# Kernel tuning notes

Measured on AMD Instinct MI355X. Metric: run time of the kernel, lower is better.

Reference implementation:

```python
import jax, jax.numpy as jnp
import numpy as np

N = 100000
NODE_DIM = 128
HIDDEN_DIM = 64
E = 625000


def setup_inputs() -> dict:
    key = jax.random.key(0)
    k_x, k_e, k_w1, k_b1, k_w2, k_b2 = jax.random.split(key, 6)
    x = jax.random.normal(k_x, (N, NODE_DIM), dtype=jnp.float32)
    edge_index = jax.random.randint(k_e, (2, E), 0, N, dtype=jnp.int64)
    # nn.Linear default init: U(-1/sqrt(fan_in), 1/sqrt(fan_in))
    lim1 = 1.0 / np.sqrt(2 * NODE_DIM)
    W1 = jax.random.uniform(k_w1, (2 * NODE_DIM, HIDDEN_DIM), minval=-lim1, maxval=lim1, dtype=jnp.float32)
    b1 = jax.random.uniform(k_b1, (HIDDEN_DIM,), minval=-lim1, maxval=lim1, dtype=jnp.float32)
    lim2 = 1.0 / np.sqrt(HIDDEN_DIM)
    W2 = jax.random.uniform(k_w2, (HIDDEN_DIM, 1), minval=-lim2, maxval=lim2, dtype=jnp.float32)
    b2 = jax.random.uniform(k_b2, (1,), minval=-lim2, maxval=lim2, dtype=jnp.float32)
    return {"x": x, "edge_index": edge_index, "W1": W1, "b1": b1, "W2": W2, "b2": b2}


def reference(x, edge_index, W1, b1, W2, b2):
    row, col = edge_index[0], edge_index[1]
    # (E, 2*node_dim) gathered edge features
    edge_attr = jnp.concatenate([x[row], x[col]], axis=-1)
    h = jax.nn.relu(edge_attr @ W1 + b1)           # (E, hidden)
    edge_mask = jax.nn.sigmoid(h @ W2 + b2)[:, 0]  # (E,)
    return edge_mask
```

## Files before the change

kernel.cpp:

```cpp
#include <hip/hip_runtime.h>
#include <hip/hip_bf16.h>

typedef unsigned short u16x8 __attribute__((ext_vector_type(8)));
typedef __bf16 bf16x8 __attribute__((ext_vector_type(8)));
typedef float f32x4 __attribute__((ext_vector_type(4)));

#define NODE_DIM 128
#define LPAD 136

__device__ __forceinline__ unsigned short f2bf(float f) {
  union { float f; unsigned int u; } v; v.f = f;
  unsigned int u = v.u;
  u += 0x7fffu + ((u >> 16) & 1u);
  return (unsigned short)(u >> 16);
}
__device__ __forceinline__ float bf2f(unsigned short s) {
  union { unsigned int u; float f; } v; v.u = ((unsigned int)s) << 16;
  return v.f;
}

__global__ void prep_wt(const float* __restrict__ W1, unsigned short* __restrict__ Wt) {
  for (int i = blockIdx.x * blockDim.x + threadIdx.x; i < 128 * 128;
       i += gridDim.x * blockDim.x) {
    int j = i >> 7, k = i & 127;
    float w = (j < 64) ? W1[k * 64 + j] : W1[(k + 128) * 64 + (j - 64)];
    Wt[i] = f2bf(w);
  }
}

__global__ __launch_bounds__(256) void gemm_pq(const float* __restrict__ x,
                                               const unsigned short* __restrict__ Wt,
                                               unsigned short* __restrict__ PQ,
                                               int n_nodes) {
  __shared__ unsigned short bs[128][LPAD];
  const int tid = threadIdx.x;

  for (int i = tid; i < 128 * 16; i += 256) {
    int j = i >> 4, c = i & 15;
    *(u16x8*)&bs[j][c * 8] = *(const u16x8*)&Wt[j * 128 + c * 8];
  }
  __syncthreads();

  const int wave = tid >> 6, lane = tid & 63;
  const int m = lane & 15, q = lane >> 4;

  #pragma unroll
  for (int step = 0; step < 2; ++step) {
    const int row0 = blockIdx.x * 128 + step * 64 + wave * 16;
    if (row0 < n_nodes) {
      const int arow = min(row0 + m, n_nodes - 1);
      const float* xr = x + (size_t)arow * NODE_DIM;

      float4 av[4][2];
      #pragma unroll
      for (int kk = 0; kk < 4; kk++) {
        av[kk][0] = *(const float4*)&xr[kk * 32 + q * 8];
        av[kk][1] = *(const float4*)&xr[kk * 32 + q * 8 + 4];
      }

      f32x4 acc[8];
      #pragma unroll
      for (int t = 0; t < 8; t++) acc[t] = f32x4{0.f, 0.f, 0.f, 0.f};

      #pragma unroll
      for (int kk = 0; kk < 4; kk++) {
        union { unsigned short s[8]; u16x8 v; } au;
        au.s[0] = f2bf(av[kk][0].x); au.s[1] = f2bf(av[kk][0].y);
        au.s[2] = f2bf(av[kk][0].z); au.s[3] = f2bf(av[kk][0].w);
        au.s[4] = f2bf(av[kk][1].x); au.s[5] = f2bf(av[kk][1].y);
        au.s[6] = f2bf(av[kk][1].z); au.s[7] = f2bf(av[kk][1].w);
        bf16x8 a = __builtin_bit_cast(bf16x8, au.v);
        #pragma unroll
        for (int t = 0; t < 8; t++) {
          bf16x8 b = __builtin_bit_cast(bf16x8,
              *(const u16x8*)&bs[t * 16 + m][kk * 32 + q * 8]);
          acc[t] = __builtin_amdgcn_mfma_f32_16x16x32_bf16(a, b, acc[t], 0, 0, 0);
        }
      }

      #pragma unroll
      for (int t = 0; t < 8; t++) {
        #pragma unroll
        for (int r = 0; r < 4; r++) {
          int gr = row0 + q * 4 + r;
          if (gr < n_nodes) PQ[(size_t)gr * 128 + t * 16 + m] = f2bf(acc[t][r]);
        }
      }
    }
  }
}

__global__ __launch_bounds__(256) void edge_mlp(const int* __restrict__ ei,
                                                const unsigned short* __restrict__ PQ,
                                                const float* __restrict__ b1,
                                                const float* __restrict__ W2,
                                                const float* __restrict__ b2,
                                                float* __restrict__ out, int E) {
  const int t = blockIdx.x * 256 + threadIdx.x;
  const int e = t >> 3, l = t & 7;
  if (e >= E) return;
  const int row = ei[e];
  const int col = ei[E + e];
  u16x8 pu = *(const u16x8*)&PQ[(size_t)row * 128 + l * 8];
  u16x8 qu = *(const u16x8*)&PQ[(size_t)col * 128 + 64 + l * 8];
  float partial = 0.f;
  #pragma unroll
  for (int i = 0; i < 8; i++) {
    float h = bf2f(pu[i]) + bf2f(qu[i]) + b1[l * 8 + i];
    h = fmaxf(h, 0.f);
    partial = fmaf(h, W2[l * 8 + i], partial);
  }
  partial += __shfl_xor(partial, 1);
  partial += __shfl_xor(partial, 2);
  partial += __shfl_xor(partial, 4);
  if (l == 0) out[e] = 1.f / (1.f + __expf(-(partial + b2[0])));
}

extern "C" void kernel_launch(void* const* d_in, const int* in_sizes, int n_in,
                              void* d_out, int out_size, void* d_ws, size_t ws_size,
                              hipStream_t stream) {
  const float* x  = (const float*)d_in[0];
  const int*   ei = (const int*)d_in[1];
  const float* W1 = (const float*)d_in[2];
  const float* b1 = (const float*)d_in[3];
  const float* W2 = (const float*)d_in[4];
  const float* b2 = (const float*)d_in[5];
  float* out = (float*)d_out;
  const int n_nodes = in_sizes[0] / NODE_DIM;
  const int E = in_sizes[1] / 2;

  unsigned short* Wt = (unsigned short*)d_ws;
  unsigned short* PQ = (unsigned short*)((char*)d_ws + 32768);

  prep_wt<<<16, 256, 0, stream>>>(W1, Wt);
  gemm_pq<<<(n_nodes + 127) / 128, 256, 0, stream>>>(x, Wt, PQ, n_nodes);
  const int egrid = (E * 8 + 255) / 256;
  edge_mlp<<<egrid, 256, 0, stream>>>(ei, PQ, b1, W2, b2, out, E);
}
```

Before: 129.0 us.

## Fuse weight prep, node GEMM and edge MLP into one cooperative kernel

Replaces the three separate launches with a single persistent cooperative kernel of 512 blocks. The phases are separated by grid-wide syncs, and the work uses grid-stride loops over node tiles and edges. This removes per-launch overhead and the idle gaps between kernels. In exchange it adds grid.sync costs and limits parallelism to a fixed resident grid, which may lower memory-level parallelism. The original three-kernel path stays as a fallback if the cooperative launch fails.

```diff
diff --git a/kernel.cpp b/kernel.cpp
--- a/kernel.cpp
+++ b/kernel.cpp
@@ -1,5 +1,8 @@
 #include <hip/hip_runtime.h>
 #include <hip/hip_bf16.h>
+#include <hip/hip_cooperative_groups.h>
+
+namespace cg = cooperative_groups;
 
 typedef unsigned short u16x8 __attribute__((ext_vector_type(8)));
 typedef __bf16 bf16x8 __attribute__((ext_vector_type(8)));
@@ -7,6 +10,7 @@
 
 #define NODE_DIM 128
 #define LPAD 136
+#define GRID_BLKS 512
 
 __device__ __forceinline__ unsigned short f2bf(float f) {
   union { float f; unsigned int u; } v; v.f = f;
@@ -17,6 +21,100 @@
 __device__ __forceinline__ float bf2f(unsigned short s) {
   union { unsigned int u; float f; } v; v.u = ((unsigned int)s) << 16;
   return v.f;
+}
+
+__global__ __launch_bounds__(256, 2) void fused(
+    const float* __restrict__ x, const int* __restrict__ ei,
+    const float* __restrict__ W1, const float* __restrict__ b1,
+    const float* __restrict__ W2, const float* __restrict__ b2,
+    float* __restrict__ out, unsigned short* __restrict__ Wt,
+    unsigned short* __restrict__ PQ, int n_nodes, int E) {
+  __shared__ unsigned short bs[128][LPAD];
+  const int tid = threadIdx.x;
+  const int nthreads = gridDim.x * 256;
+  cg::grid_group grid = cg::this_grid();
+
+  for (int i = blockIdx.x * 256 + tid; i < 128 * 128; i += nthreads) {
+    int j = i >> 7, k = i & 127;
+    float w = (j < 64) ? W1[k * 64 + j] : W1[(k + 128) * 64 + (j - 64)];
+    Wt[i] = f2bf(w);
+  }
+  __threadfence();
+  grid.sync();
+
+  for (int i = tid; i < 128 * 16; i += 256) {
+    int j = i >> 4, c = i & 15;
+    *(u16x8*)&bs[j][c * 8] = *(const u16x8*)&Wt[j * 128 + c * 8];
+  }
+  __syncthreads();
+
+  const int wave = tid >> 6, lane = tid & 63;
+  const int m = lane & 15, q = lane >> 4;
+  const int ntiles = (n_nodes + 63) / 64;
+
+  for (int tile = blockIdx.x; tile < ntiles; tile += gridDim.x) {
+    const int row0 = tile * 64 + wave * 16;
+    const int arow = min(row0 + m, n_nodes - 1);
+    const float* xr = x + (size_t)arow * NODE_DIM;
+
+    float4 av[4][2];
+    #pragma unroll
+    for (int kk = 0; kk < 4; kk++) {
+      av[kk][0] = *(const float4*)&xr[kk * 32 + q * 8];
+      av[kk][1] = *(const float4*)&xr[kk * 32 + q * 8 + 4];
+    }
+
+    f32x4 acc[8];
+    #pragma unroll
+    for (int t = 0; t < 8; t++) acc[t] = f32x4{0.f, 0.f, 0.f, 0.f};
+
+    #pragma unroll
+    for (int kk = 0; kk < 4; kk++) {
+      union { unsigned short s[8]; u16x8 v; } au;
+      au.s[0] = f2bf(av[kk][0].x); au.s[1] = f2bf(av[kk][0].y);
+      au.s[2] = f2bf(av[kk][0].z); au.s[3] = f2bf(av[kk][0].w);
+      au.s[4] = f2bf(av[kk][1].x); au.s[5] = f2bf(av[kk][1].y);
+      au.s[6] = f2bf(av[kk][1].z); au.s[7] = f2bf(av[kk][1].w);
+      bf16x8 a = __builtin_bit_cast(bf16x8, au.v);
+      #pragma unroll
+      for (int t = 0; t < 8; t++) {
+        bf16x8 b = __builtin_bit_cast(bf16x8,
+            *(const u16x8*)&bs[t * 16 + m][kk * 32 + q * 8]);
+        acc[t] = __builtin_amdgcn_mfma_f32_16x16x32_bf16(a, b, acc[t], 0, 0, 0);
+      }
+    }
+
+    #pragma unroll
+    for (int t = 0; t < 8; t++) {
+      #pragma unroll
+      for (int r = 0; r < 4; r++) {
+        int gr = row0 + q * 4 + r;
+        if (gr < n_nodes) PQ[(size_t)gr * 128 + t * 16 + m] = f2bf(acc[t][r]);
+      }
+    }
+  }
+  __threadfence();
+  grid.sync();
+
+  const int l = tid & 7;
+  for (int idx = blockIdx.x * 256 + tid; (idx >> 3) < E; idx += nthreads) {
+    const int e = idx >> 3;
+    const int row = ei[e];
+    const int col = ei[E + e];
+    u16x8 pu = *(const u16x8*)&PQ[(size_t)row * 128 + l * 8];
+    u16x8 qu = *(const u16x8*)&PQ[(size_t)col * 128 + 64 + l * 8];
+    float partial = 0.f;
+    #pragma unroll
+    for (int i = 0; i < 8; i++) {
+      float h = bf2f(pu[i]) + bf2f(qu[i]) + b1[l * 8 + i];
+      h = fmaxf(h, 0.f);
+      partial = fmaf(h, W2[l * 8 + i], partial);
+    }
+    partial += __shfl_xor(partial, 1);
+    partial += __shfl_xor(partial, 2);
+    partial += __shfl_xor(partial, 4);
+    if (l == 0) out[e] = 1.f / (1.f + __expf(-(partial + b2[0])));
+  }
 }
 
 __global__ void prep_wt(const float* __restrict__ W1, unsigned short* __restrict__ Wt) {
@@ -34,34 +132,28 @@
                                                int n_nodes) {
   __shared__ unsigned short bs[128][LPAD];
   const int tid = threadIdx.x;
-
   for (int i = tid; i < 128 * 16; i += 256) {
     int j = i >> 4, c = i & 15;
     *(u16x8*)&bs[j][c * 8] = *(const u16x8*)&Wt[j * 128 + c * 8];
   }
   __syncthreads();
-
   const int wave = tid >> 6, lane = tid & 63;
   const int m = lane & 15, q = lane >> 4;
-
   #pragma unroll
   for (int step = 0; step < 2; ++step) {
     const int row0 = blockIdx.x * 128 + step * 64 + wave * 16;
     if (row0 < n_nodes) {
       const int arow = min(row0 + m, n_nodes - 1);
       const float* xr = x + (size_t)arow * NODE_DIM;
-
       float4 av[4][2];
       #pragma unroll
       for (int kk = 0; kk < 4; kk++) {
         av[kk][0] = *(const float4*)&xr[kk * 32 + q * 8];
         av[kk][1] = *(const float4*)&xr[kk * 32 + q * 8 + 4];
       }
-
       f32x4 acc[8];
       #pragma unroll
       for (int t = 0; t < 8; t++) acc[t] = f32x4{0.f, 0.f, 0.f, 0.f};
-
       #pragma unroll
       for (int kk = 0; kk < 4; kk++) {
         union { unsigned short s[8]; u16x8 v; } au;
@@ -77,7 +169,6 @@
           acc[t] = __builtin_amdgcn_mfma_f32_16x16x32_bf16(a, b, acc[t], 0, 0, 0);
         }
       }
-
       #pragma unroll
       for (int t = 0; t < 8; t++) {
         #pragma unroll
@@ -126,14 +217,21 @@
   const float* W2 = (const float*)d_in[4];
   const float* b2 = (const float*)d_in[5];
   float* out = (float*)d_out;
-  const int n_nodes = in_sizes[0] / NODE_DIM;
-  const int E = in_sizes[1] / 2;
+  int n_nodes = in_sizes[0] / NODE_DIM;
+  int E = in_sizes[1] / 2;
 
   unsigned short* Wt = (unsigned short*)d_ws;
   unsigned short* PQ = (unsigned short*)((char*)d_ws + 32768);
 
-  prep_wt<<<16, 256, 0, stream>>>(W1, Wt);
-  gemm_pq<<<(n_nodes + 127) / 128, 256, 0, stream>>>(x, Wt, PQ, n_nodes);
-  const int egrid = (E * 8 + 255) / 256;
-  edge_mlp<<<egrid, 256, 0, stream>>>(ei, PQ, b1, W2, b2, out, E);
-}
+  void* args[] = {(void*)&x, (void*)&ei, (void*)&W1, (void*)&b1, (void*)&W2,
+                  (void*)&b2, (void*)&out, (void*)&Wt, (void*)&PQ,
+                  (void*)&n_nodes, (void*)&E};
+  hipError_t err = hipLaunchCooperativeKernel(
+      reinterpret_cast<void*>(fused), dim3(GRID_BLKS), dim3(256), args, 0, stream);
+  if (err != hipSuccess) {
+    prep_wt<<<16, 256, 0, stream>>>(W1, Wt);
+    gemm_pq<<<(n_nodes + 127) / 128, 256, 0, stream>>>(x, Wt, PQ, n_nodes);
+    const int egrid = (E * 8 + 255) / 256;
+    edge_mlp<<<egrid, 256, 0, stream>>>(ei, PQ, b1, W2, b2, out, E);
+  }
+}
```

Result: slower. 336.2 us (+160.7%).
